# Performance work log

Hardware: AMD Instinct MI355X
Metric: run time of the kernel (lower is better)

The kernel has to match this reference:

```python
import jax, jax.numpy as jnp
import numpy as np

NUM_HEADS = 16
NEG = -1e10


def setup_inputs() -> dict:
    key = jax.random.key(0)
    ks = jax.random.split(key, 5)
    S, E = 2048, 2048
    scale_in = 1.0 / np.sqrt(E)
    return {
        "x": jax.random.normal(ks[0], (S, E), dtype=jnp.float32),
        "W_attn": jax.random.normal(ks[1], (E, 3 * E), dtype=jnp.float32) * scale_in,
        "b_attn": jax.random.normal(ks[2], (3 * E,), dtype=jnp.float32) * 0.02,
        "W_proj": jax.random.normal(ks[3], (E, E), dtype=jnp.float32) * scale_in,
        "b_proj": jax.random.normal(ks[4], (E,), dtype=jnp.float32) * 0.02,
    }


def reference(x, W_attn, b_attn, W_proj, b_proj):
    S, E = x.shape
    H = NUM_HEADS
    D = E // H
    # c_attn: [S, 3E]
    h = x @ W_attn + b_attn
    # view(S, 3, -1).transpose(0,1) -> [3, S, E]; then view(3, S, H, D).transpose(1,2) -> [3, H, S, D]
    qkv = h.reshape(S, 3, E).transpose(1, 0, 2)          # [3, S, E]
    q, k, v = qkv.reshape(3, S, H, D).transpose(0, 2, 1, 3)  # each [H, S, D]
    # causal mask: (1 - tril) * -1e10, added before softmax
    mask = (1.0 - jnp.tril(jnp.ones((S, S), dtype=x.dtype))) * NEG
    scores = jnp.einsum("hsd,htd->hst", q, k) / jnp.sqrt(jnp.asarray(D, dtype=x.dtype))
    attn = jax.nn.softmax(scores + mask, axis=-1)
    out_heads = jnp.einsum("hst,htd->hsd", attn, v)      # [H, S, D]
    # hstack over heads == transpose to [S, H, D] then flatten to [S, E]
    concat = out_heads.transpose(1, 0, 2).reshape(S, E)
    out = concat @ W_proj + b_proj
    # current_cache = (k, v) pre-head-split: [S, E] each
    return out, qkv[1], qkv[2]
```

## Files before the change

### kernel.cpp

```cpp
#include <hip/hip_runtime.h>
#include <hip/hip_bf16.h>
#include <stdint.h>

#define S_DIM 2048
#define E_DIM 2048
#define H_NUM 16
#define D_HEAD 128
#define N3E 6144

typedef __attribute__((ext_vector_type(8))) short short8;
typedef __attribute__((ext_vector_type(4))) float f32x4;
typedef __attribute__((ext_vector_type(8))) unsigned short ushort8;

__device__ __forceinline__ unsigned short f32_to_bf16_bits(float f) {
    __hip_bfloat16 b = __float2bfloat16(f);
    unsigned short u;
    __builtin_memcpy(&u, &b, 2);
    return u;
}
__device__ __forceinline__ float bf16_bits_to_f32(unsigned short u) {
    unsigned int v = ((unsigned int)u) << 16;
    float f;
    __builtin_memcpy(&f, &v, 4);
    return f;
}

__global__ void k_convert(const float* __restrict__ in, __hip_bfloat16* __restrict__ out, int n) {
    int i = (blockIdx.x * 256 + threadIdx.x) * 8;
    if (i >= n) return;
    float4 a = *(const float4*)(in + i);
    float4 b = *(const float4*)(in + i + 4);
    ushort8 o;
    o[0] = f32_to_bf16_bits(a.x);
    o[1] = f32_to_bf16_bits(a.y);
    o[2] = f32_to_bf16_bits(a.z);
    o[3] = f32_to_bf16_bits(a.w);
    o[4] = f32_to_bf16_bits(b.x);
    o[5] = f32_to_bf16_bits(b.y);
    o[6] = f32_to_bf16_bits(b.z);
    o[7] = f32_to_bf16_bits(b.w);
    *(ushort8*)(out + i) = o;
}

__global__ void k_transpose_convert(const float* __restrict__ in, __hip_bfloat16* __restrict__ out,
                                    int R, int C) {
    __shared__ float tile[32][33];
    int c0 = blockIdx.x * 32, r0 = blockIdx.y * 32;
    int tx = threadIdx.x, ty = threadIdx.y;
#pragma unroll
    for (int i = 0; i < 4; ++i) {
        int r = r0 + ty + i * 8;
        tile[ty + i * 8][tx] = in[(size_t)r * C + c0 + tx];
    }
    __syncthreads();
#pragma unroll
    for (int i = 0; i < 4; ++i) {
        int c = c0 + ty + i * 8;
        out[(size_t)c * R + r0 + tx] = __float2bfloat16(tile[tx][ty + i * 8]);
    }
}

__global__ void k_transpose_v(const __hip_bfloat16* __restrict__ qkv, __hip_bfloat16* __restrict__ vT) {
    __shared__ __hip_bfloat16 tile[32][33];
    int c0 = blockIdx.x * 32, t0 = blockIdx.y * 32;
    int tx = threadIdx.x, ty = threadIdx.y;
#pragma unroll
    for (int i = 0; i < 4; ++i) {
        int t = t0 + ty + i * 8;
        tile[ty + i * 8][tx] = qkv[(size_t)t * N3E + 2 * E_DIM + c0 + tx];
    }
    __syncthreads();
#pragma unroll
    for (int i = 0; i < 4; ++i) {
        int c = c0 + ty + i * 8;
        vT[(size_t)c * S_DIM + t0 + tx] = tile[tx][ty + i * 8];
    }
}

template <int EPI>
__global__ __launch_bounds__(512, 2) void k_gemm256(const __hip_bfloat16* __restrict__ A,
                                                    const __hip_bfloat16* __restrict__ Bt,
                                                    const float* __restrict__ bias,
                                                    float* __restrict__ outF,
                                                    __hip_bfloat16* __restrict__ outB,
                                                    int M, int N, int K) {
    __shared__ __hip_bfloat16 As[4][256 * 32];
    __shared__ __hip_bfloat16 Bs[4][256 * 32];

    const int tid = threadIdx.x;
    const int w = tid >> 6, lane = tid & 63;
    const int lg = lane >> 4, l16 = lane & 15;
    const int wr = w >> 2, wc = w & 3;
    const int m0 = blockIdx.y * 256, n0 = blockIdx.x * 256;
    const int NT = K >> 5;

    const int srow = tid >> 2;
    const int scol = ((tid & 3) ^ ((tid >> 3) & 3)) * 8;
    const __hip_bfloat16* aB = A + (size_t)(m0 + srow) * K + scol;
    const __hip_bfloat16* bB = Bt + (size_t)(n0 + srow) * K + scol;
    const size_t rstep = (size_t)128 * K;

#define STAGE(u, p)                                                                                   \
    do {                                                                                              \
        __builtin_amdgcn_global_load_lds(                                                             \
            (const __attribute__((address_space(1))) void*)(aB + (p) * rstep + (u) * 32),             \
            (__attribute__((address_space(3))) void*)(&As[(u) & 3][(p) * 4096 + tid * 8]), 16, 0, 0); \
        __builtin_amdgcn_global_load_lds(                                                             \
            (const __attribute__((address_space(1))) void*)(bB + (p) * rstep + (u) * 32),             \
            (__attribute__((address_space(3))) void*)(&Bs[(u) & 3][(p) * 4096 + tid * 8]), 16, 0, 0); \
    } while (0)

    f32x4 acc[8][4];
#pragma unroll
    for (int i = 0; i < 8; ++i)
#pragma unroll
        for (int j = 0; j < 4; ++j) acc[i][j] = {0.f, 0.f, 0.f, 0.f};

    STAGE(0, 0); STAGE(0, 1);
    STAGE(1, 0); STAGE(1, 1);
    STAGE(2, 0); STAGE(2, 1);
    asm volatile("s_waitcnt vmcnt(8)" ::: "memory");
    __builtin_amdgcn_s_barrier();

    short8 af[4], bf[4];
    for (int t = 0; t < NT; ++t) {
        const int cur = t & 3;
        const int u = t + 3;
#pragma unroll
        for (int i = 0; i < 4; ++i) {
            int arow = wr * 128 + i * 16 + l16;
            af[i] = *(const short8*)&As[cur][arow * 32 + ((lg ^ ((arow >> 1) & 3)) * 8)];
            int brow = wc * 64 + i * 16 + l16;
            bf[i] = *(const short8*)&Bs[cur][brow * 32 + ((lg ^ ((brow >> 1) & 3)) * 8)];
        }
        if (u < NT) STAGE(u, 0);
        __builtin_amdgcn_s_barrier();
        __builtin_amdgcn_s_setprio(1);
#pragma unroll
        for (int mi = 0; mi < 4; ++mi)
#pragma unroll
            for (int ni = 0; ni < 4; ++ni)
                acc[mi][ni] = __builtin_amdgcn_mfma_f32_16x16x32_bf16(af[mi], bf[ni], acc[mi][ni], 0, 0, 0);
        __builtin_amdgcn_s_setprio(0);
        __builtin_amdgcn_s_barrier();
#pragma unroll
        for (int i = 0; i < 4; ++i) {
            int arow = wr * 128 + 64 + i * 16 + l16;
            af[i] = *(const short8*)&As[cur][arow * 32 + ((lg ^ ((arow >> 1) & 3)) * 8)];
        }
        if (u < NT) STAGE(u, 1);
        __builtin_amdgcn_s_barrier();
        __builtin_amdgcn_s_setprio(1);
#pragma unroll
        for (int mi = 0; mi < 4; ++mi)
#pragma unroll
            for (int ni = 0; ni < 4; ++ni)
                acc[4 + mi][ni] = __builtin_amdgcn_mfma_f32_16x16x32_bf16(af[mi], bf[ni], acc[4 + mi][ni], 0, 0, 0);
        __builtin_amdgcn_s_setprio(0);
        __builtin_amdgcn_sched_barrier(0);
        if (t < NT - 3)
            asm volatile("s_waitcnt vmcnt(8)" ::: "memory");
        else if (t == NT - 3)
            asm volatile("s_waitcnt vmcnt(4)" ::: "memory");
        else if (t == NT - 2)
            asm volatile("s_waitcnt vmcnt(0)" ::: "memory");
        __builtin_amdgcn_sched_barrier(0);
        __builtin_amdgcn_s_barrier();
    }
#undef STAGE

    const size_t OFF_K = (size_t)S_DIM * E_DIM;
    const size_t OFF_V = 2 * (size_t)S_DIM * E_DIM;
#pragma unroll
    for (int ni = 0; ni < 4; ++ni) {
        int jcol = n0 + wc * 64 + ni * 16 + l16;
        float bj = bias[jcol];
#pragma unroll
        for (int mi = 0; mi < 8; ++mi) {
#pragma unroll
            for (int r = 0; r < 4; ++r) {
                int s = m0 + wr * 128 + mi * 16 + lg * 4 + r;
                float v = acc[mi][ni][r] + bj;
                if (EPI == 1) {
                    outB[(size_t)s * N + jcol] = __float2bfloat16(v);
                    if (jcol >= 2 * E_DIM) {
                        outF[OFF_V + (size_t)s * E_DIM + (jcol - 2 * E_DIM)] = v;
                    } else if (jcol >= E_DIM) {
                        outF[OFF_K + (size_t)s * E_DIM + (jcol - E_DIM)] = v;
                    }
                } else {
                    outF[(size_t)s * N + jcol] = v;
                }
            }
        }
    }
}

template <int EPI>
__global__ __launch_bounds__(256) void k_gemm(const __hip_bfloat16* __restrict__ A,
                                              const __hip_bfloat16* __restrict__ Bt,
                                              const float* __restrict__ bias,
                                              float* __restrict__ outF,
                                              __hip_bfloat16* __restrict__ outB,
                                              int M, int N, int K) {
    __shared__ __hip_bfloat16 As[128 * 32];
    __shared__ __hip_bfloat16 Bs[128 * 32];
    const int w = threadIdx.x >> 6, lane = threadIdx.x & 63;
    const int lg = lane >> 4, l16 = lane & 15;
    const int wr = w >> 1, wc = w & 1;
    const int m0 = blockIdx.y * 128, n0 = blockIdx.x * 128;

    f32x4 acc[4][4];
#pragma unroll
    for (int i = 0; i < 4; ++i)
#pragma unroll
        for (int j = 0; j < 4; ++j) acc[i][j] = {0.f, 0.f, 0.f, 0.f};

    const int scol = (lane & 3) * 8;

    for (int k0 = 0; k0 < K; k0 += 32) {
#pragma unroll
        for (int j = 0; j < 2; ++j) {
            int c = w * 2 + j;
            int row = c * 16 + (lane >> 2);
            const __hip_bfloat16* ga = A + (size_t)(m0 + row) * K + k0 + scol;
            const __hip_bfloat16* gb = Bt + (size_t)(n0 + row) * K + k0 + scol;
            __builtin_amdgcn_global_load_lds((const __attribute__((address_space(1))) void*)ga,
                                             (__attribute__((address_space(3))) void*)(As + c * 512),
                                             16, 0, 0);
            __builtin_amdgcn_global_load_lds((const __attribute__((address_space(1))) void*)gb,
                                             (__attribute__((address_space(3))) void*)(Bs + c * 512),
                                             16, 0, 0);
        }
        __syncthreads();
        short8 af[4], bfr[4];
#pragma unroll
        for (int mi = 0; mi < 4; ++mi)
            af[mi] = *(const short8*)&As[(wr * 64 + mi * 16 + l16) * 32 + lg * 8];
#pragma unroll
        for (int ni = 0; ni < 4; ++ni)
            bfr[ni] = *(const short8*)&Bs[(wc * 64 + ni * 16 + l16) * 32 + lg * 8];
#pragma unroll
        for (int mi = 0; mi < 4; ++mi)
#pragma unroll
            for (int ni = 0; ni < 4; ++ni)
                acc[mi][ni] = __builtin_amdgcn_mfma_f32_16x16x32_bf16(af[mi], bfr[ni], acc[mi][ni], 0, 0, 0);
        __syncthreads();
    }

    const size_t OFF_K = (size_t)S_DIM * E_DIM;
    const size_t OFF_V = 2 * (size_t)S_DIM * E_DIM;
#pragma unroll
    for (int ni = 0; ni < 4; ++ni) {
        int jcol = n0 + wc * 64 + ni * 16 + l16;
        float bj = bias[jcol];
#pragma unroll
        for (int mi = 0; mi < 4; ++mi) {
#pragma unroll
            for (int r = 0; r < 4; ++r) {
                int s = m0 + wr * 64 + mi * 16 + lg * 4 + r;
                float v = acc[mi][ni][r] + bj;
                if (EPI == 1) {
                    outB[(size_t)s * N + jcol] = __float2bfloat16(v);
                    if (jcol >= 2 * E_DIM) {
                        outF[OFF_V + (size_t)s * E_DIM + (jcol - 2 * E_DIM)] = v;
                    } else if (jcol >= E_DIM) {
                        outF[OFF_K + (size_t)s * E_DIM + (jcol - E_DIM)] = v;
                    }
                } else {
                    outF[(size_t)s * N + jcol] = v;
                }
            }
        }
    }
}

__global__ __launch_bounds__(256) void k_attn(const __hip_bfloat16* __restrict__ qkv,
                                              const __hip_bfloat16* __restrict__ vT,
                                              __hip_bfloat16* __restrict__ concat,
                                              __hip_bfloat16* __restrict__ Ob,
                                              float* __restrict__ ml) {
    const int h = blockIdx.y;
    const int xs = 47 - (int)blockIdx.x;
    int x, tstart, tend, chunk = 0;
    bool split;
    if (xs < 16) {
        x = xs; tstart = 0; tend = x + 1; split = false;
    } else {
        int idx = xs - 16;
        x = 16 + (idx >> 1);
        chunk = idx & 1;
        int L = x + 1, half = L >> 1;
        tstart = chunk ? half : 0;
        tend = chunk ? L : half;
        split = true;
    }
    const int q0 = x * 64;
    const int tid = threadIdx.x;
    const int w = tid >> 6, lane = tid & 63;
    const int lg = lane >> 4, l16 = lane & 15;
    const int sbase = q0 + w * 16;
    const float scale = 0.08838834764831845f;
    const float FIXM = 8.0f;

    __shared__ __hip_bfloat16 Ks[2][64 * 128];
    __shared__ __hip_bfloat16 Vs[2][128 * 64];
    __shared__ __hip_bfloat16 plds[4][16 * 84];

    short8 qa[4];
#pragma unroll
    for (int kc = 0; kc < 4; ++kc)
        qa[kc] = *(const short8*)&qkv[(size_t)(sbase + l16) * N3E + h * D_HEAD + kc * 32 + lg * 8];

    short8 ones;
#pragma unroll
    for (int j = 0; j < 8; ++j) ones[j] = (short)0x3F80;

    f32x4 O[8];
#pragma unroll
    for (int i = 0; i < 8; ++i) O[i] = {0.f, 0.f, 0.f, 0.f};
    f32x4 accL = {0.f, 0.f, 0.f, 0.f};

    auto stage = [&](int buf, int it) {
        const int t0 = it * 64;
#pragma unroll
        for (int j = 0; j < 4; ++j) {
            int kr = j * 16 + w * 4 + (lane >> 4);
            int ks16 = (lane & 15) ^ (kr & 7);
            const __hip_bfloat16* gk = qkv + (size_t)(t0 + kr) * N3E + E_DIM + h * D_HEAD + ks16 * 8;
            __builtin_amdgcn_global_load_lds((const __attribute__((address_space(1))) void*)gk,
                                             (__attribute__((address_space(3))) void*)(&Ks[buf][j * 2048 + w * 512]),
                                             16, 0, 0);
            int vd = j * 32 + w * 8 + (lane >> 3);
            int vs16 = (lane & 7) ^ (vd & 7);
            const __hip_bfloat16* gv = vT + (size_t)(h * D_HEAD + vd) * S_DIM + t0 + vs16 * 8;
            __builtin_amdgcn_global_load_lds((const __attribute__((address_space(1))) void*)gv,
                                             (__attribute__((address_space(3))) void*)(&Vs[buf][j * 2048 + w * 512]),
                                             16, 0, 0);
        }
    };

    stage(0, tstart);
    int cur = 0;

    for (int it = tstart; it < tend; ++it) {
        const int t0 = it * 64;
        __syncthreads();
        if (it + 1 < tend) stage(cur ^ 1, it + 1);
        const bool diag = (t0 == q0);

        f32x4 sc[4];
        __builtin_amdgcn_s_setprio(1);
#pragma unroll
        for (int f = 0; f < 4; ++f) {
            sc[f] = {0.f, 0.f, 0.f, 0.f};
            int r = f * 16 + l16;
#pragma unroll
            for (int kc = 0; kc < 4; ++kc) {
                int ce = (kc * 32 + lg * 8) ^ ((r & 7) << 3);
                short8 kb = *(const short8*)&Ks[cur][r * 128 + ce];
                sc[f] = __builtin_amdgcn_mfma_f32_16x16x32_bf16(qa[kc], kb, sc[f], 0, 0, 0);
            }
        }
        __builtin_amdgcn_s_setprio(0);

#pragma unroll
        for (int f = 0; f < 4; ++f) {
#pragma unroll
            for (int r = 0; r < 4; ++r) {
                float v = sc[f][r] * scale - FIXM;
                if (diag) {
                    int t = t0 + f * 16 + l16;
                    int s = sbase + lg * 4 + r;
                    if (t > s) v = -1e30f;
                }
                sc[f][r] = __expf(v);
            }
        }

#pragma unroll
        for (int f = 0; f < 4; ++f)
#pragma unroll
            for (int r = 0; r < 4; ++r)
                plds[w][(lg * 4 + r) * 84 + f * 16 + l16] = __float2bfloat16(sc[f][r]);
        short8 pa[2];
#pragma unroll
        for (int tc = 0; tc < 2; ++tc)
            pa[tc] = *(const short8*)&plds[w][l16 * 84 + tc * 32 + lg * 8];

        __builtin_amdgcn_s_setprio(1);
        accL = __builtin_amdgcn_mfma_f32_16x16x32_bf16(pa[0], ones, accL, 0, 0, 0);
        accL = __builtin_amdgcn_mfma_f32_16x16x32_bf16(pa[1], ones, accL, 0, 0, 0);
#pragma unroll
        for (int f2 = 0; f2 < 8; ++f2) {
            int d = f2 * 16 + l16;
#pragma unroll
            for (int tc = 0; tc < 2; ++tc) {
                int ce = (tc * 32 + lg * 8) ^ ((d & 7) << 3);
                short8 vb = *(const short8*)&Vs[cur][d * 64 + ce];
                O[f2] = __builtin_amdgcn_mfma_f32_16x16x32_bf16(pa[tc], vb, O[f2], 0, 0, 0);
            }
        }
        __builtin_amdgcn_s_setprio(0);
        cur ^= 1;
    }

    if (!split) {
#pragma unroll
        for (int f2 = 0; f2 < 8; ++f2) {
#pragma unroll
            for (int r = 0; r < 4; ++r) {
                int s = sbase + lg * 4 + r;
                float v = O[f2][r] / accL[r];
                concat[(size_t)s * E_DIM + h * D_HEAD + f2 * 16 + l16] = __float2bfloat16(v);
            }
        }
    } else {
        const int sub = (h * 16 + (x - 16)) * 2 + chunk;
#pragma unroll
        for (int f2 = 0; f2 < 8; ++f2) {
#pragma unroll
            for (int r = 0; r < 4; ++r) {
                int row = w * 16 + lg * 4 + r;
                Ob[(size_t)sub * 8192 + row * 128 + f2 * 16 + l16] = __float2bfloat16(O[f2][r]);
            }
        }
        if (l16 == 0) {
#pragma unroll
            for (int r = 0; r < 4; ++r) {
                int row = w * 16 + lg * 4 + r;
                ml[((size_t)sub * 64 + row) * 2 + 0] = FIXM;
                ml[((size_t)sub * 64 + row) * 2 + 1] = accL[r];
            }
        }
    }
}

__global__ __launch_bounds__(256) void k_combine(const __hip_bfloat16* __restrict__ Ob,
                                                 const float* __restrict__ ml,
                                                 __hip_bfloat16* __restrict__ concat) {
    const int xx = blockIdx.x;
    const int h = blockIdx.y;
    const int tid = threadIdx.x;
    const int row = tid >> 2;
    const int d0 = (tid & 3) * 32;
    const int sub0 = (h * 16 + xx) * 2, sub1 = sub0 + 1;
    const float m0 = ml[((size_t)sub0 * 64 + row) * 2 + 0];
    const float l0 = ml[((size_t)sub0 * 64 + row) * 2 + 1];
    const float m1 = ml[((size_t)sub1 * 64 + row) * 2 + 0];
    const float l1 = ml[((size_t)sub1 * 64 + row) * 2 + 1];
    const float M = fmaxf(m0, m1);
    const float w0 = __expf(m0 - M), w1 = __expf(m1 - M);
    const float inv = 1.f / (w0 * l0 + w1 * l1);
    const int s = (xx + 16) * 64 + row;
#pragma unroll
    for (int j = 0; j < 32; j += 8) {
        ushort8 a = *(const ushort8*)&Ob[(size_t)sub0 * 8192 + row * 128 + d0 + j];
        ushort8 b = *(const ushort8*)&Ob[(size_t)sub1 * 8192 + row * 128 + d0 + j];
        ushort8 o;
#pragma unroll
        for (int q = 0; q < 8; ++q) {
            float fa = bf16_bits_to_f32(a[q]);
            float fb = bf16_bits_to_f32(b[q]);
            o[q] = f32_to_bf16_bits((w0 * fa + w1 * fb) * inv);
        }
        *(ushort8*)&concat[(size_t)s * E_DIM + h * D_HEAD + d0 + j] = o;
    }
}

extern "C" void kernel_launch(void* const* d_in, const int* in_sizes, int n_in,
                              void* d_out, int out_size, void* d_ws, size_t ws_size,
                              hipStream_t stream) {
    const float* x = (const float*)d_in[0];
    const float* W_attn = (const float*)d_in[1];
    const float* b_attn = (const float*)d_in[2];
    const float* W_proj = (const float*)d_in[3];
    const float* b_proj = (const float*)d_in[4];
    float* out = (float*)d_out;

    __hip_bfloat16* xb = (__hip_bfloat16*)d_ws;
    __hip_bfloat16* WaT = xb + (size_t)S_DIM * E_DIM;
    __hip_bfloat16* WpT = WaT + (size_t)N3E * E_DIM;
    __hip_bfloat16* qkvb = WpT + (size_t)E_DIM * E_DIM;
    __hip_bfloat16* vT = qkvb + (size_t)S_DIM * N3E;
    __hip_bfloat16* concat = xb;
    __hip_bfloat16* Ob = WaT;
    float* ml = (float*)(WaT + (size_t)512 * 8192);

    k_convert<<<dim3((S_DIM * E_DIM) / (256 * 8)), dim3(256), 0, stream>>>(x, xb, S_DIM * E_DIM);
    k_transpose_convert<<<dim3(N3E / 32, E_DIM / 32), dim3(32, 8), 0, stream>>>(W_attn, WaT, E_DIM, N3E);
    k_transpose_convert<<<dim3(E_DIM / 32, E_DIM / 32), dim3(32, 8), 0, stream>>>(W_proj, WpT, E_DIM, E_DIM);
    k_gemm256<1><<<dim3(N3E / 256, S_DIM / 256), dim3(512), 0, stream>>>(xb, WaT, b_attn, out, qkvb,
                                                                         S_DIM, N3E, E_DIM);
    k_transpose_v<<<dim3(E_DIM / 32, S_DIM / 32), dim3(32, 8), 0, stream>>>(qkvb, vT);
    k_attn<<<dim3(48, H_NUM), dim3(256), 0, stream>>>(qkvb, vT, concat, Ob, ml);
    k_combine<<<dim3(16, H_NUM), dim3(256), 0, stream>>>(Ob, ml, concat);
    k_gemm<0><<<dim3(E_DIM / 128, S_DIM / 128), dim3(256), 0, stream>>>(concat, WpT, b_proj, out,
                                                                        nullptr, S_DIM, E_DIM, E_DIM);
}
```

Measured before the change: 217.6 us.

## Pipeline projection GEMM with 4-stage LDS ring, swizzle block order, trim barriers

The output-projection GEMM is replaced by a 128x128 kernel that uses a 4-deep global_load_lds ring buffer with swizzled LDS columns and vmcnt-based waits, so loads overlap with MFMA work instead of syncing twice per k-step. Both GEMMs now launch a 1D grid and remap block indices so consecutive blocks are spread across XCD-sized chunks, aiming at better L2 locality. The QKV GEMM issues both halves of the next stage together and drops two of its in-loop barriers. This reduces synchronisation but relies on the ring depth to keep the remaining barrier sufficient for correctness.

```diff
diff --git a/kernel.cpp b/kernel.cpp
--- a/kernel.cpp
+++ b/kernel.cpp
@@ -91,7 +91,11 @@
     const int w = tid >> 6, lane = tid & 63;
     const int lg = lane >> 4, l16 = lane & 15;
     const int wr = w >> 2, wc = w & 3;
-    const int m0 = blockIdx.y * 256, n0 = blockIdx.x * 256;
+    const int ntx = N >> 8;
+    const int chunk = ((M >> 8) * ntx) >> 3;
+    const int lin = blockIdx.x;
+    const int swz = (lin & 7) * chunk + (lin >> 3);
+    const int m0 = (swz / ntx) << 8, n0 = (swz % ntx) << 8;
     const int NT = K >> 5;
 
     const int srow = tid >> 2;
@@ -133,8 +137,7 @@
             int brow = wc * 64 + i * 16 + l16;
             bf[i] = *(const short8*)&Bs[cur][brow * 32 + ((lg ^ ((brow >> 1) & 3)) * 8)];
         }
-        if (u < NT) STAGE(u, 0);
-        __builtin_amdgcn_s_barrier();
+        if (u < NT) { STAGE(u, 0); STAGE(u, 1); }
         __builtin_amdgcn_s_setprio(1);
 #pragma unroll
         for (int mi = 0; mi < 4; ++mi)
@@ -142,14 +145,11 @@
             for (int ni = 0; ni < 4; ++ni)
                 acc[mi][ni] = __builtin_amdgcn_mfma_f32_16x16x32_bf16(af[mi], bf[ni], acc[mi][ni], 0, 0, 0);
         __builtin_amdgcn_s_setprio(0);
-        __builtin_amdgcn_s_barrier();
 #pragma unroll
         for (int i = 0; i < 4; ++i) {
             int arow = wr * 128 + 64 + i * 16 + l16;
             af[i] = *(const short8*)&As[cur][arow * 32 + ((lg ^ ((arow >> 1) & 3)) * 8)];
         }
-        if (u < NT) STAGE(u, 1);
-        __builtin_amdgcn_s_barrier();
         __builtin_amdgcn_s_setprio(1);
 #pragma unroll
         for (int mi = 0; mi < 4; ++mi)
@@ -197,18 +197,41 @@
 }
 
 template <int EPI>
-__global__ __launch_bounds__(256) void k_gemm(const __hip_bfloat16* __restrict__ A,
-                                              const __hip_bfloat16* __restrict__ Bt,
-                                              const float* __restrict__ bias,
-                                              float* __restrict__ outF,
-                                              __hip_bfloat16* __restrict__ outB,
-                                              int M, int N, int K) {
-    __shared__ __hip_bfloat16 As[128 * 32];
-    __shared__ __hip_bfloat16 Bs[128 * 32];
-    const int w = threadIdx.x >> 6, lane = threadIdx.x & 63;
+__global__ __launch_bounds__(256, 2) void k_gemm128(const __hip_bfloat16* __restrict__ A,
+                                                    const __hip_bfloat16* __restrict__ Bt,
+                                                    const float* __restrict__ bias,
+                                                    float* __restrict__ outF,
+                                                    __hip_bfloat16* __restrict__ outB,
+                                                    int M, int N, int K) {
+    __shared__ __hip_bfloat16 As[4][128 * 32];
+    __shared__ __hip_bfloat16 Bs[4][128 * 32];
+
+    const int tid = threadIdx.x;
+    const int w = tid >> 6, lane = tid & 63;
     const int lg = lane >> 4, l16 = lane & 15;
     const int wr = w >> 1, wc = w & 1;
-    const int m0 = blockIdx.y * 128, n0 = blockIdx.x * 128;
+    const int ntx = N >> 7;
+    const int chunk = ((M >> 7) * ntx) >> 3;
+    const int lin = blockIdx.x;
+    const int swz = (lin & 7) * chunk + (lin >> 3);
+    const int m0 = (swz / ntx) << 7, n0 = (swz % ntx) << 7;
+    const int NT = K >> 5;
+
+    const int srow = tid >> 2;
+    const int scol = ((tid & 3) ^ ((tid >> 3) & 3)) * 8;
+    const __hip_bfloat16* aB = A + (size_t)(m0 + srow) * K + scol;
+    const __hip_bfloat16* bB = Bt + (size_t)(n0 + srow) * K + scol;
+    const size_t rstep = (size_t)64 * K;
+
+#define STG(u, p)                                                                                     \
+    do {                                                                                              \
+        __builtin_amdgcn_global_load_lds(                                                             \
+            (const __attribute__((address_space(1))) void*)(aB + (p) * rstep + (u) * 32),             \
+            (__attribute__((address_space(3))) void*)(&As[(u) & 3][(p) * 2048 + tid * 8]), 16, 0, 0); \
+        __builtin_amdgcn_global_load_lds(                                                             \
+            (const __attribute__((address_space(1))) void*)(bB + (p) * rstep + (u) * 32),             \
+            (__attribute__((address_space(3))) void*)(&Bs[(u) & 3][(p) * 2048 + tid * 8]), 16, 0, 0); \
+    } while (0)
 
     f32x4 acc[4][4];
 #pragma unroll
@@ -216,37 +239,42 @@
 #pragma unroll
         for (int j = 0; j < 4; ++j) acc[i][j] = {0.f, 0.f, 0.f, 0.f};
 
-    const int scol = (lane & 3) * 8;
-
-    for (int k0 = 0; k0 < K; k0 += 32) {
-#pragma unroll
-        for (int j = 0; j < 2; ++j) {
-            int c = w * 2 + j;
-            int row = c * 16 + (lane >> 2);
-            const __hip_bfloat16* ga = A + (size_t)(m0 + row) * K + k0 + scol;
-            const __hip_bfloat16* gb = Bt + (size_t)(n0 + row) * K + k0 + scol;
-            __builtin_amdgcn_global_load_lds((const __attribute__((address_space(1))) void*)ga,
-                                             (__attribute__((address_space(3))) void*)(As + c * 512),
-                                             16, 0, 0);
-            __builtin_amdgcn_global_load_lds((const __attribute__((address_space(1))) void*)gb,
-                                             (__attribute__((address_space(3))) void*)(Bs + c * 512),
-                                             16, 0, 0);
-        }
-        __syncthreads();
-        short8 af[4], bfr[4];
-#pragma unroll
-        for (int mi = 0; mi < 4; ++mi)
-            af[mi] = *(const short8*)&As[(wr * 64 + mi * 16 + l16) * 32 + lg * 8];
-#pragma unroll
-        for (int ni = 0; ni < 4; ++ni)
-            bfr[ni] = *(const short8*)&Bs[(wc * 64 + ni * 16 + l16) * 32 + lg * 8];
+    STG(0, 0); STG(0, 1);
+    STG(1, 0); STG(1, 1);
+    STG(2, 0); STG(2, 1);
+    asm volatile("s_waitcnt vmcnt(8)" ::: "memory");
+    __builtin_amdgcn_s_barrier();
+
+    short8 af[4], bfr[4];
+    for (int t = 0; t < NT; ++t) {
+        const int cur = t & 3;
+        const int u = t + 3;
+#pragma unroll
+        for (int i = 0; i < 4; ++i) {
+            int arow = wr * 64 + i * 16 + l16;
+            af[i] = *(const short8*)&As[cur][arow * 32 + ((lg ^ ((arow >> 1) & 3)) * 8)];
+            int brow = wc * 64 + i * 16 + l16;
+            bfr[i] = *(const short8*)&Bs[cur][brow * 32 + ((lg ^ ((brow >> 1) & 3)) * 8)];
+        }
+        if (u < NT) { STG(u, 0); STG(u, 1); }
+        __builtin_amdgcn_s_setprio(1);
 #pragma unroll
         for (int mi = 0; mi < 4; ++mi)
 #pragma unroll
             for (int ni = 0; ni < 4; ++ni)
                 acc[mi][ni] = __builtin_amdgcn_mfma_f32_16x16x32_bf16(af[mi], bfr[ni], acc[mi][ni], 0, 0, 0);
-        __syncthreads();
-    }
+        __builtin_amdgcn_s_setprio(0);
+        __builtin_amdgcn_sched_barrier(0);
+        if (t < NT - 3)
+            asm volatile("s_waitcnt vmcnt(8)" ::: "memory");
+        else if (t == NT - 3)
+            asm volatile("s_waitcnt vmcnt(4)" ::: "memory");
+        else if (t == NT - 2)
+            asm volatile("s_waitcnt vmcnt(0)" ::: "memory");
+        __builtin_amdgcn_sched_barrier(0);
+        __builtin_amdgcn_s_barrier();
+    }
+#undef STG
 
     const size_t OFF_K = (size_t)S_DIM * E_DIM;
     const size_t OFF_V = 2 * (size_t)S_DIM * E_DIM;
@@ -490,11 +518,10 @@
     k_convert<<<dim3((S_DIM * E_DIM) / (256 * 8)), dim3(256), 0, stream>>>(x, xb, S_DIM * E_DIM);
     k_transpose_convert<<<dim3(N3E / 32, E_DIM / 32), dim3(32, 8), 0, stream>>>(W_attn, WaT, E_DIM, N3E);
     k_transpose_convert<<<dim3(E_DIM / 32, E_DIM / 32), dim3(32, 8), 0, stream>>>(W_proj, WpT, E_DIM, E_DIM);
-    k_gemm256<1><<<dim3(N3E / 256, S_DIM / 256), dim3(512), 0, stream>>>(xb, WaT, b_attn, out, qkvb,
-                                                                         S_DIM, N3E, E_DIM);
+    k_gemm256<1><<<dim3(192), dim3(512), 0, stream>>>(xb, WaT, b_attn, out, qkvb, S_DIM, N3E, E_DIM);
     k_transpose_v<<<dim3(E_DIM / 32, S_DIM / 32), dim3(32, 8), 0, stream>>>(qkvb, vT);
     k_attn<<<dim3(48, H_NUM), dim3(256), 0, stream>>>(qkvb, vT, concat, Ob, ml);
     k_combine<<<dim3(16, H_NUM), dim3(256), 0, stream>>>(Ob, ml, concat);
-    k_gemm<0><<<dim3(E_DIM / 128, S_DIM / 128), dim3(256), 0, stream>>>(concat, WpT, b_proj, out,
-                                                                        nullptr, S_DIM, E_DIM, E_DIM);
-}
+    k_gemm128<0><<<dim3(256), dim3(256), 0, stream>>>(concat, WpT, b_proj, out, nullptr,
+                                                      S_DIM, E_DIM, E_DIM);
+}
```

Measured after the change: 206.3 us. 1.05x faster.
